# Kernel tuning notes

Measured on AMD Instinct MI355X. Metric: run time of the kernel, lower is better.

Reference implementation:

```python
import jax, jax.numpy as jnp
import jax.numpy.linalg as jnla
import numpy as np
from jax import lax
from jax.scipy.special import polygamma, betainc
import jax.scipy.stats as jaxstats

N, K, L = 2000, 10, 10000   # samples, covariates, cis variants
R = 200                     # max_perm_direct
MAX_ITER_BETA = 100         # max_iter_beta
STEPSIZE, TOL = 1.0, 1e-3


def setup_inputs() -> dict:
    key = jax.random.key(0)
    kx, ky, kg, kp = jax.random.split(key, 4)
    return {
        "X": jax.random.normal(kx, (N, K), jnp.float32),
        "y": jax.random.normal(ky, (N,), jnp.float32),
        "G": jax.random.normal(kg, (N, L), jnp.float32),
        "obs_p": jax.random.uniform(kp, (L,), jnp.float32),
        "offset_eta": jnp.zeros((N,), jnp.float32),
        "seed": 0,
    }


def _beta_loglik(params, p):
    return jnp.sum(jaxstats.beta.logpdf(p, params[0], params[1]))


def _info_and_christoffel(params, n_obs):
    k, n = params[0], params[1]
    pg_1k = polygamma(1, k); pg_1n = polygamma(1, n); pg_1kn = polygamma(1, k + n)
    pg_2k = polygamma(2, k); pg_2n = polygamma(2, n); pg_2kn = polygamma(2, k + n)
    i_kn = -pg_1kn
    i_k = pg_1k + i_kn
    i_n = pg_1n + i_kn
    info_mat = -n_obs * jnp.array([[i_k, i_kn], [i_kn, i_n]])
    i_kkn = pg_1n * pg_2kn
    i_k = -pg_1n * pg_2k + i_kkn + pg_1kn * pg_2k
    i_knn = i_kkn - pg_1kn * pg_2n
    i_nnk = pg_1k * pg_2kn
    i_nkk = i_nnk - pg_1kn * pg_2k
    i_n = -pg_1k * pg_2n + i_nnk + pg_1kn * pg_2n
    scale = -pg_1k * pg_1n + (pg_1k + pg_1n) * pg_1kn
    sec_gamma = 0.5 * jnp.array([[[i_k, i_kkn], [i_kkn, i_knn]],
                                 [[i_nkk, i_nnk], [i_nnk, i_n]]]) / scale
    return info_mat, sec_gamma


def _infer_beta(p_perm, init, max_iter):
    # Newton-Raphson with Christoffel correction; fixed-length scan with an
    # 'active' freeze mask (reverse-differentiable equivalent of the while_loop).
    score_fn = jax.grad(_beta_loglik)
    n_obs = p_perm.shape[0]

    def step(carry, _):
        old_lik, diff, num_iter, old_param = carry
        active = jnp.logical_and(jnp.abs(diff) > TOL, num_iter <= max_iter)
        info_mat, gamma = _info_and_christoffel(old_param, n_obs)
        direction = jnla.solve(info_mat, score_fn(old_param, p_perm))
        adjustment = jnp.einsum('cab,a,b->c', gamma, direction, direction)
        new_param = old_param - STEPSIZE * direction - 0.5 * STEPSIZE ** 2 * adjustment
        new_lik = _beta_loglik(new_param, p_perm)
        new_diff = old_lik - new_lik
        carry = (jnp.where(active, new_lik, old_lik),
                 jnp.where(active, new_diff, diff),
                 jnp.where(active, num_iter + 1, num_iter),
                 jnp.where(active, new_param, old_param))
        return carry, None

    init_c = (jnp.float32(10000.0), jnp.float32(1000.0), jnp.int32(0), init)
    (lik, diff, num_iters, params), _ = lax.scan(step, init_c, None, length=max_iter + 1)
    converged = jnp.logical_and(jnp.abs(diff) < TOL, num_iters <= max_iter).astype(jnp.float32)
    return jnp.array([params[0], params[1], converged])


def _beta_perm(X, y, G, obs_p, offset_eta, seed):
    key = jax.random.key(seed)
    XtX = X.T @ X                               # [K,K]
    Gt = G - X @ jnla.solve(XtX, X.T @ G)       # variants residualized on covariates [N,L]
    gg = jnp.sum(Gt * Gt, axis=0)               # [L]
    dof = N - K - 1

    def perm_step(k, _):
        k, p_key = jax.random.split(k)
        y_p = jax.random.permutation(p_key, y, axis=0) - offset_eta
        yt = y_p - X @ jnla.solve(XtX, X.T @ y_p)   # residualized phenotype [N]
        gy = Gt.T @ y_p                             # == Gt.T @ yt since Gt perp X
        beta = gy / gg
        rss = jnp.sum(yt * yt) - beta * beta * gg   # per-variant residual SS [L]
        se = jnp.sqrt(rss / dof / gg)
        return k, jnp.max(jnp.abs(beta / se))

    _, TS = lax.scan(perm_step, key, None, length=R)          # [R] lead |Z| stats
    p_perm = 1.0 - jaxstats.chi2.cdf(jnp.square(TS), 1.0)     # pval_from_Zstat, dof=1
    p_mean, p_var = jnp.mean(p_perm), jnp.var(p_perm)
    k_init = p_mean * (p_mean * (1.0 - p_mean) / p_var - 1.0)
    n_init = k_init * (1.0 / p_mean - 1.0)
    beta_res = _infer_beta(p_perm, jnp.array([k_init, n_init]), MAX_ITER_BETA)
    # _calc_adjp_beta: Beta CDF of the strongest nominal p-value
    adj_p = betainc(beta_res[0], beta_res[1], jnp.min(obs_p))
    return adj_p, beta_res


def reference(X, y, G, obs_p, offset_eta, seed):
    return _beta_perm(X, y, G, obs_p, offset_eta, seed)
```

## Files before the change

### kernel.cpp

```cpp
#include <hip/hip_runtime.h>
#include <stdint.h>

#ifndef JAX_THREEFRY_PARTITIONABLE
#define JAX_THREEFRY_PARTITIONABLE 1
#endif

#define N_SAMP 2000
#define L_VAR  10000
#define R_PERM 200
#define DOF_D  1989.0

#define KPAD   2048
#define LPAD   10048
#define RPAD   256

#define OFF_PKEYS  0UL
#define OFF_MI     1664UL
#define OFF_MINP   2464UL
#define OFF_XT     2560UL
#define OFF_XTGP   82560UL
#define OFF_GGP    2082560UL
#define OFF_GG     2282560UL
#define OFF_YTY    2322560UL
#define OFF_S      2323392UL
#define OFF_YT     2324224UL
#define WS_OLD     3924224UL
#define OFF_GGP2   82560UL
#define OFF_RGG    725632UL
#define OFF_YHI    2324224UL
#define OFF_XTGP2  3924224UL
#define OFF_YLO    10354944UL
#define OFF_GTHI   11403520UL
#define OFF_GTLO   52560128UL
#define WS_BIG     95186432UL

typedef __attribute__((ext_vector_type(8))) short short8v;
typedef __attribute__((ext_vector_type(4))) float float4v;

__device__ __forceinline__ uint32_t rotl32(uint32_t v, int d) {
  return (v << d) | (v >> (32 - d));
}
__device__ __forceinline__ uint2 tf2(uint32_t k0, uint32_t k1, uint32_t x0, uint32_t x1) {
  uint32_t ks2 = k0 ^ k1 ^ 0x1BD11BDAu;
  x0 += k0; x1 += k1;
#define TF4(a,b,c,d) \
  x0 += x1; x1 = rotl32(x1,a); x1 ^= x0; \
  x0 += x1; x1 = rotl32(x1,b); x1 ^= x0; \
  x0 += x1; x1 = rotl32(x1,c); x1 ^= x0; \
  x0 += x1; x1 = rotl32(x1,d); x1 ^= x0;
  TF4(13,15,26,6)  x0 += k1;  x1 += ks2 + 1u;
  TF4(17,29,16,24) x0 += ks2; x1 += k0 + 2u;
  TF4(13,15,26,6)  x0 += k0;  x1 += k1 + 3u;
  TF4(17,29,16,24) x0 += k1;  x1 += ks2 + 4u;
  TF4(13,15,26,6)  x0 += ks2; x1 += k0 + 5u;
#undef TF4
  return make_uint2(x0, x1);
}

__device__ __forceinline__ void gen_pkeys(const int* seedp, unsigned* pkeys) {
  uint32_t khi = 0u, klo = (uint32_t)(*seedp);
  for (int r = 0; r < R_PERM; ++r) {
#if JAX_THREEFRY_PARTITIONABLE
    uint2 pk = tf2(khi, klo, 0u, 1u);
    uint2 nk = tf2(khi, klo, 0u, 0u);
#else
    uint2 t0 = tf2(khi, klo, 0u, 2u);
    uint2 t1 = tf2(khi, klo, 1u, 3u);
    uint2 nk = make_uint2(t0.x, t1.x);
    uint2 pk = make_uint2(t0.y, t1.y);
#endif
    pkeys[2 * r] = pk.x; pkeys[2 * r + 1] = pk.y;
    khi = nk.x; klo = nk.y;
  }
}

__device__ __forceinline__ double breduce_add(double v, double* red, int tid) {
  red[tid] = v; __syncthreads();
  for (int off = 128; off > 0; off >>= 1) {
    if (tid < off) red[tid] += red[tid + off];
    __syncthreads();
  }
  double r = red[0]; __syncthreads();
  return r;
}

__device__ double dg_digamma(double x) {
  if (!(x > 0.0)) return __builtin_nan("");
  double r = 0.0;
  while (x < 8.0) { r -= 1.0 / x; x += 1.0; }
  double t = 1.0 / x, t2 = t * t;
  double ser = t2 * (1.0/12.0 - t2*(1.0/120.0 - t2*(1.0/252.0 - t2*(1.0/240.0 - t2*(1.0/132.0)))));
  return r + log(x) - 0.5 * t - ser;
}
__device__ double dg_trigamma(double x) {
  if (!(x > 0.0)) return __builtin_nan("");
  double r = 0.0;
  while (x < 8.0) { r += 1.0 / (x * x); x += 1.0; }
  double t = 1.0 / x, t2 = t * t;
  double P = 1.0/6.0 - t2*(1.0/30.0 - t2*(1.0/42.0 - t2*(1.0/30.0 - t2*(5.0/66.0))));
  return r + t + 0.5 * t2 + t * t2 * P;
}
__device__ double dg_tetragamma(double x) {
  if (!(x > 0.0)) return __builtin_nan("");
  double r = 0.0;
  while (x < 8.0) { r -= 2.0 / (x * x * x); x += 1.0; }
  double t = 1.0 / x, t2 = t * t;
  double Q = 1.0 + t + 0.5*t2 - t2*t2*(1.0/6.0 - t2*(1.0/6.0 - t2*(3.0/10.0)));
  return r - t2 * Q;
}
__device__ double betacf_d(double a, double b, double x) {
  const double FPMIN = 1e-300, EPS = 3e-16;
  double qab = a + b, qap = a + 1.0, qam = a - 1.0;
  double c = 1.0, d = 1.0 - qab * x / qap;
  if (fabs(d) < FPMIN) d = FPMIN;
  d = 1.0 / d; double h = d;
  for (int m = 1; m <= 300; ++m) {
    int m2 = 2 * m;
    double aa = m * (b - m) * x / ((qam + m2) * (a + m2));
    d = 1.0 + aa * d; if (fabs(d) < FPMIN) d = FPMIN;
    c = 1.0 + aa / c; if (fabs(c) < FPMIN) c = FPMIN;
    d = 1.0 / d; double del = d * c; h *= del;
    aa = -(a + m) * (qab + m) * x / ((a + m2) * (qap + m2));
    d = 1.0 + aa * d; if (fabs(d) < FPMIN) d = FPMIN;
    c = 1.0 + aa / c; if (fabs(c) < FPMIN) c = FPMIN;
    d = 1.0 / d; del = d * c; h *= del;
    if (fabs(del - 1.0) < EPS) break;
  }
  return h;
}
__device__ double betainc_d(double a, double b, double x) {
  if (!(x > 0.0)) return 0.0;
  if (x >= 1.0) return 1.0;
  double lnbt = lgamma(a + b) - lgamma(a) - lgamma(b) + a * log(x) + b * log1p(-x);
  double bt = exp(lnbt);
  if (x < (a + 1.0) / (a + b + 2.0)) return bt * betacf_d(a, b, x) / a;
  else return 1.0 - bt * betacf_d(b, a, 1.0 - x) / b;
}

__device__ __forceinline__ void fill_keys(unsigned long long* arr, uint32_t kx, uint32_t ky,
                                          int tid, int nthr) {
#if JAX_THREEFRY_PARTITIONABLE
  for (int i = tid; i < 2048; i += nthr) {
    if (i < 2000) {
      uint2 o = tf2(kx, ky, 0u, (uint32_t)i);
      uint32_t bits = o.x ^ o.y;
      arr[i] = (((unsigned long long)bits) << 11) | (unsigned long long)i;
    } else {
      arr[i] = ~0ull;
    }
  }
#else
  for (int j = tid; j < 1024; j += nthr) {
    if (j < 1000) {
      uint2 o = tf2(kx, ky, (uint32_t)j, (uint32_t)(1000 + j));
      arr[j]        = (((unsigned long long)o.x) << 11) | (unsigned long long)j;
      arr[1000 + j] = (((unsigned long long)o.y) << 11) | (unsigned long long)(1000 + j);
    }
  }
  for (int i = 2000 + tid; i < 2048; i += nthr) arr[i] = ~0ull;
#endif
}

__device__ __forceinline__ void tri_ab(int q, int& a, int& b) {
  int aa = 0, rem = q;
  while (rem >= 10 - aa) { rem -= 10 - aa; ++aa; }
  a = aa; b = aa + rem;
}

__device__ __forceinline__ void bf16split(float f, unsigned short& h, unsigned short& l) {
  unsigned u = __float_as_uint(f);
  h = (unsigned short)(u >> 16);
  float rem = f - __uint_as_float(u & 0xFFFF0000u);
  l = (unsigned short)(__float_as_uint(rem) >> 16);
}

__global__ __launch_bounds__(256) void k1_setup(
    const float* __restrict__ X, const float* __restrict__ obs_p,
    float* __restrict__ Xt, double* __restrict__ Mi, float* __restrict__ minp,
    unsigned short* __restrict__ yhi, unsigned short* __restrict__ ylo) {
  int tid = threadIdx.x;
  if (blockIdx.x == 0) {
    __shared__ double wsum[4][55];
    __shared__ double xtx_sh[55];
    __shared__ double A[10][21];
    __shared__ int piv_sh;
    __shared__ double pv_sh;
    int wave = tid >> 6, lane = tid & 63;

    double acc[55];
    #pragma unroll
    for (int q = 0; q < 55; ++q) acc[q] = 0.0;
    for (int i = tid; i < N_SAMP; i += 256) {
      float xv[10];
      #pragma unroll
      for (int k = 0; k < 5; ++k) {
        float2 t2 = *(const float2*)(X + i * 10 + 2 * k);
        xv[2 * k] = t2.x; xv[2 * k + 1] = t2.y;
      }
      int q = 0;
      #pragma unroll
      for (int a = 0; a < 10; ++a)
        #pragma unroll
        for (int b = a; b < 10; ++b)
          acc[q++] += (double)xv[a] * (double)xv[b];
    }
    #pragma unroll
    for (int q = 0; q < 55; ++q) {
      double v = acc[q];
      #pragma unroll
      for (int off = 32; off > 0; off >>= 1) v += __shfl_xor(v, off, 64);
      if (lane == 0) wsum[wave][q] = v;
    }
    __syncthreads();
    if (tid < 55) xtx_sh[tid] = wsum[0][tid] + wsum[1][tid] + wsum[2][tid] + wsum[3][tid];
    __syncthreads();

    if (tid < 200) {
      int r = tid / 20, j = tid % 20;
      double v;
      if (j < 10) {
        int a = r < j ? r : j;
        int b = r < j ? j : r;
        int q = 10 * a - a * (a - 1) / 2 + (b - a);
        v = xtx_sh[q];
      } else {
        v = (j - 10 == r) ? 1.0 : 0.0;
      }
      A[r][j] = v;
    }
    __syncthreads();
    int r_ = tid / 20, j_ = tid % 20;
    bool in200 = (tid < 200);
    for (int c = 0; c < 10; ++c) {
      if (tid == 0) {
        int piv = c; double best = fabs(A[c][c]);
        for (int r2 = c + 1; r2 < 10; ++r2)
          if (fabs(A[r2][c]) > best) { best = fabs(A[r2][c]); piv = r2; }
        piv_sh = piv;
      }
      __syncthreads();
      int piv = piv_sh;
      if (piv != c && tid < 20) {
        double t = A[c][tid]; A[c][tid] = A[piv][tid]; A[piv][tid] = t;
      }
      __syncthreads();
      if (tid == 0) pv_sh = A[c][c];
      __syncthreads();
      if (tid < 20) A[c][tid] *= (1.0 / pv_sh);
      __syncthreads();
      double f = 0.0, acj = 0.0;
      bool act = in200 && (r_ != c);
      if (act) { f = A[r_][c]; acj = A[c][j_]; }
      __syncthreads();
      if (act) A[r_][j_] -= f * acj;
      __syncthreads();
    }
    if (tid < 100) Mi[tid] = A[tid / 10][10 + (tid % 10)];
  } else if (blockIdx.x == 1) {
    __shared__ float redf[256];
    float m = 1e30f;
    for (int i = tid; i < L_VAR; i += 256) m = fminf(m, obs_p[i]);
    redf[tid] = m; __syncthreads();
    for (int off = 128; off > 0; off >>= 1) {
      if (tid < off) redf[tid] = fminf(redf[tid], redf[tid + off]);
      __syncthreads();
    }
    if (tid == 0) *minp = redf[0];
  } else if (blockIdx.x == 2) {
    for (int idx = tid; idx < 10 * N_SAMP; idx += 256) {
      int k = idx / N_SAMP, i = idx - k * N_SAMP;
      Xt[idx] = X[i * 10 + k];
    }
  } else {
    if (yhi) {
      int row = R_PERM + (blockIdx.x - 3);
      size_t base = (size_t)row * KPAD;
      for (int i = tid; i < KPAD; i += 256) {
        yhi[base + i] = 0;
        ylo[base + i] = 0;
      }
    }
  }
}

__global__ __launch_bounds__(256) void k2_xtg(
    const float* __restrict__ G, const float* __restrict__ X,
    const int* __restrict__ seedp, float* __restrict__ XtGp,
    float* __restrict__ GGp, unsigned* __restrict__ pkeys) {
  if (blockIdx.x == 40) {
    if (blockIdx.y == 0 && threadIdx.x == 0) gen_pkeys(seedp, pkeys);
    return;
  }
  int l = blockIdx.x * 256 + threadIdx.x;
  bool valid = (l < L_VAR);
  int i0 = blockIdx.y * 400;
  float acc[10];
  #pragma unroll
  for (int k = 0; k < 10; ++k) acc[k] = 0.f;
  float g2 = 0.f;
  for (int i = i0; i < i0 + 400; ++i) {
    float g = valid ? G[(size_t)i * L_VAR + l] : 0.f;
    #pragma unroll
    for (int k = 0; k < 10; ++k) acc[k] = fmaf(g, X[i * 10 + k], acc[k]);
    g2 = fmaf(g, g, g2);
  }
  if (valid) {
    int part = blockIdx.y;
    #pragma unroll
    for (int k = 0; k < 10; ++k)
      XtGp[((size_t)part * 10 + k) * L_VAR + l] = acc[k];
    GGp[(size_t)part * L_VAR + l] = g2;
  }
}

__global__ __launch_bounds__(256) void k2t_pass(
    const float* __restrict__ G, const float* __restrict__ X,
    const int* __restrict__ seedp,
    unsigned short* __restrict__ GTHI, unsigned short* __restrict__ GTLO,
    float* __restrict__ XtGp2, float* __restrict__ GGp2,
    unsigned* __restrict__ pkeys) {
  if (blockIdx.x == 157) {
    if (blockIdx.y == 0 && threadIdx.x < 2) {
      int t = threadIdx.x;
      uint32_t khi = 0u, klo = (uint32_t)(*seedp);
#if JAX_THREEFRY_PARTITIONABLE
      for (int r = 0; r < R_PERM; ++r) {
        uint2 res = tf2(khi, klo, 0u, (uint32_t)t);
        if (t == 1) { pkeys[2 * r] = res.x; pkeys[2 * r + 1] = res.y; }
        khi = __shfl(res.x, 0, 64);
        klo = __shfl(res.y, 0, 64);
      }
#else
      if (t == 0) gen_pkeys(seedp, pkeys);
#endif
    }
    return;
  }
  __shared__ float T[128][69];
  __shared__ float Xsh[128][10];
  int tid = threadIdx.x;
  int l0 = blockIdx.x * 64, i0 = blockIdx.y * 128;
  for (int it = 0; it < 8; ++it) {
    int fi = it * 256 + tid;
    int row = fi >> 4, c4 = (fi & 15) * 4;
    int i = i0 + row, l = l0 + c4;
    float4 v = make_float4(0.f, 0.f, 0.f, 0.f);
    if (i < N_SAMP && l + 3 < L_VAR) v = *(const float4*)(G + (size_t)i * L_VAR + l);
    T[row][c4 + 0] = v.x; T[row][c4 + 1] = v.y; T[row][c4 + 2] = v.z; T[row][c4 + 3] = v.w;
  }
  for (int q = 0; q < 5; ++q) {
    int idx = q * 256 + tid;
    if (idx < 1280) {
      int row = idx / 10, k = idx - row * 10;
      int i = i0 + row;
      Xsh[row][k] = (i < N_SAMP) ? X[i * 10 + k] : 0.f;
    }
  }
  __syncthreads();
  {
    int w = tid >> 6, lam = tid & 63;
    int half = lam >> 5, i4 = (lam & 31) * 4;
    for (int g = 0; g < 8; ++g) {
      int lloc = g * 8 + w * 2 + half;
      float fv[4];
      fv[0] = T[i4 + 0][lloc]; fv[1] = T[i4 + 1][lloc];
      fv[2] = T[i4 + 2][lloc]; fv[3] = T[i4 + 3][lloc];
      ushort4 hv, lv;
      bf16split(fv[0], hv.x, lv.x);
      bf16split(fv[1], hv.y, lv.y);
      bf16split(fv[2], hv.z, lv.z);
      bf16split(fv[3], hv.w, lv.w);
      size_t idx = (size_t)(l0 + lloc) * KPAD + i0 + i4;
      *(ushort4*)(GTHI + idx) = hv;
      *(ushort4*)(GTLO + idx) = lv;
    }
  }
  int lc = tid & 63, iq = tid >> 6;
  float accx[10];
  #pragma unroll
  for (int k = 0; k < 10; ++k) accx[k] = 0.f;
  float g2 = 0.f;
  for (int j = 0; j < 32; ++j) {
    int i = iq * 32 + j;
    float tv = T[i][lc];
    g2 = fmaf(tv, tv, g2);
    #pragma unroll
    for (int k = 0; k < 10; ++k) accx[k] = fmaf(tv, Xsh[i][k], accx[k]);
  }
  __syncthreads();
  float* scr = &T[0][0];
  #pragma unroll
  for (int k = 0; k < 10; ++k) scr[(iq * 64 + lc) * 10 + k] = accx[k];
  scr[2560 + iq * 64 + lc] = g2;
  __syncthreads();
  for (int idx = tid; idx < 640; idx += 256) {
    int l = idx / 10, k = idx - l * 10;
    float t = scr[(0 * 64 + l) * 10 + k] + scr[(1 * 64 + l) * 10 + k]
            + scr[(2 * 64 + l) * 10 + k] + scr[(3 * 64 + l) * 10 + k];
    XtGp2[((size_t)blockIdx.y * 10 + k) * LPAD + l0 + l] = t;
  }
  if (tid < 64) {
    float s4 = scr[2560 + tid] + scr[2560 + 64 + tid] + scr[2560 + 128 + tid] + scr[2560 + 192 + tid];
    GGp2[(size_t)blockIdx.y * LPAD + l0 + tid] = s4;
  }
}

__global__ __launch_bounds__(256) void k3_gg(
    const float* __restrict__ XtGp, const float* __restrict__ GGp,
    const double* __restrict__ Mi, float* __restrict__ gg) {
  int l = blockIdx.x * 256 + threadIdx.x;
  if (l >= L_VAR) return;
  double t[10]; double g2 = 0.0;
  #pragma unroll
  for (int k = 0; k < 10; ++k) t[k] = 0.0;
  for (int part = 0; part < 5; ++part) {
    #pragma unroll
    for (int k = 0; k < 10; ++k)
      t[k] += (double)XtGp[((size_t)part * 10 + k) * L_VAR + l];
    g2 += (double)GGp[(size_t)part * L_VAR + l];
  }
  double corr = 0.0;
  #pragma unroll
  for (int k = 0; k < 10; ++k) {
    double a = 0.0;
    #pragma unroll
    for (int j = 0; j < 10; ++j) a += Mi[k * 10 + j] * t[j];
    corr += a * t[k];
  }
  gg[l] = (float)(g2 - corr);
}

__global__ __launch_bounds__(256) void k3t_gg(
    const float* __restrict__ XtGp2, const float* __restrict__ GGp2,
    const double* __restrict__ Mi, float* __restrict__ gg, float* __restrict__ rgg) {
  int l = blockIdx.x * 256 + threadIdx.x;
  if (l >= LPAD) return;
  double t[10]; double g2 = 0.0;
  #pragma unroll
  for (int k = 0; k < 10; ++k) t[k] = 0.0;
  for (int part = 0; part < 16; ++part) {
    #pragma unroll
    for (int k = 0; k < 10; ++k)
      t[k] += (double)XtGp2[((size_t)part * 10 + k) * LPAD + l];
    g2 += (double)GGp2[(size_t)part * LPAD + l];
  }
  double corr = 0.0;
  #pragma unroll
  for (int k = 0; k < 10; ++k) {
    double a = 0.0;
    #pragma unroll
    for (int j = 0; j < 10; ++j) a += Mi[k * 10 + j] * t[j];
    corr += a * t[k];
  }
  double v = g2 - corr;
  if (l < L_VAR) {
    gg[l] = (float)v;
    rgg[l] = (v > 0.0) ? (float)(1.0 / v) : 0.f;
  } else {
    rgg[l] = 0.f;
  }
}

__global__ __launch_bounds__(1024) void k4_perm(
    const float* __restrict__ y, const float* __restrict__ offs,
    const float* __restrict__ Xt, const unsigned* __restrict__ pkeys,
    const double* __restrict__ Mi, float* __restrict__ Yt,
    float* __restrict__ yty, unsigned* __restrict__ s,
    unsigned short* __restrict__ yhi, unsigned short* __restrict__ ylo) {
  __shared__ unsigned long long arrA[2048];
  __shared__ unsigned long long arrB[2048];
  __shared__ float yp[2000];
  __shared__ double redL[16][10];
  __shared__ double wf[10];
  __shared__ double red16[16];
  __shared__ double mvd[10];
  __shared__ unsigned ksh[4];
  const int NT = 1024;
  int r = blockIdx.x, tid = threadIdx.x;
  int wid = tid >> 6, lane = tid & 63;

  if (tid == 0) {
    uint32_t phi = pkeys[2 * r], plo = pkeys[2 * r + 1];
#if JAX_THREEFRY_PARTITIONABLE
    uint2 sub1 = tf2(phi, plo, 0u, 1u);
    uint2 key1 = tf2(phi, plo, 0u, 0u);
    uint2 sub2 = tf2(key1.x, key1.y, 0u, 1u);
#else
    uint2 a0 = tf2(phi, plo, 0u, 2u), a1 = tf2(phi, plo, 1u, 3u);
    uint2 key1 = make_uint2(a0.x, a1.x);
    uint2 sub1 = make_uint2(a0.y, a1.y);
    uint2 b0 = tf2(key1.x, key1.y, 0u, 2u), b1 = tf2(key1.x, key1.y, 1u, 3u);
    uint2 sub2 = make_uint2(b0.y, b1.y);
#endif
    ksh[0] = sub1.x; ksh[1] = sub1.y; ksh[2] = sub2.x; ksh[3] = sub2.y;
  }
  __syncthreads();
  uint32_t s1x = ksh[0], s1y = ksh[1], s2x = ksh[2], s2y = ksh[3];

  fill_keys(arrA, s1x, s1y, tid, NT);
  fill_keys(arrB, s2x, s2y, tid, NT);

  for (int size = 2; size <= 2048; size <<= 1) {
    for (int stride = size >> 1; stride > 0; stride >>= 1) {
      __syncthreads();
      int i = 2 * tid - (tid & (stride - 1));
      int j = i + stride;
      bool up = ((i & size) == 0);
      unsigned long long a = arrA[i], b = arrA[j];
      unsigned long long c = arrB[i], d = arrB[j];
      bool swA = up ? (a > b) : (a < b);
      bool swB = up ? (c > d) : (c < d);
      if (swA) { arrA[i] = b; arrA[j] = a; }
      if (swB) { arrB[i] = d; arrB[j] = c; }
    }
  }
  __syncthreads();

  for (int i = tid; i < N_SAMP; i += NT) {
    int s2i = (int)(arrB[i] & 2047u);
    int fin = (int)(arrA[s2i] & 2047u);
    yp[i] = y[fin] - offs[i];
  }
  __syncthreads();

  double wloc[10];
  #pragma unroll
  for (int k = 0; k < 10; ++k) wloc[k] = 0.0;
  for (int i = tid; i < N_SAMP; i += NT) {
    double v = (double)yp[i];
    #pragma unroll
    for (int k = 0; k < 10; ++k) wloc[k] += (double)Xt[k * N_SAMP + i] * v;
  }
  #pragma unroll
  for (int k = 0; k < 10; ++k) {
    double v = wloc[k];
    #pragma unroll
    for (int off = 32; off > 0; off >>= 1) v += __shfl_xor(v, off, 64);
    if (lane == 0) redL[wid][k] = v;
  }
  __syncthreads();
  if (tid < 10) {
    double t = 0.0;
    for (int w2 = 0; w2 < 16; ++w2) t += redL[w2][tid];
    wf[tid] = t;
  }
  __syncthreads();
  if (tid < 10) {
    double m = 0.0;
    #pragma unroll
    for (int k = 0; k < 10; ++k) m += Mi[tid * 10 + k] * wf[k];
    mvd[tid] = m;
  }
  __syncthreads();

  double acc = 0.0;
  for (int i = tid; i < N_SAMP; i += NT) {
    double d = (double)yp[i];
    #pragma unroll
    for (int k = 0; k < 10; ++k) d -= (double)Xt[k * N_SAMP + i] * mvd[k];
    float v = (float)d;
    if (Yt) Yt[(size_t)r * N_SAMP + i] = v;
    yp[i] = v;
    acc += (double)v * (double)v;
  }
  #pragma unroll
  for (int off = 32; off > 0; off >>= 1) acc += __shfl_xor(acc, off, 64);
  if (lane == 0) red16[wid] = acc;
  __syncthreads();
  if (tid == 0) {
    double tot = 0.0;
    for (int w2 = 0; w2 < 16; ++w2) tot += red16[w2];
    yty[r] = (float)tot;
    s[r] = 0u;
  }

  __syncthreads();
  if (yhi) {
    for (int i = tid; i < KPAD; i += NT) {
      float v = (i < N_SAMP) ? yp[i] : 0.f;
      unsigned short h, l;
      bf16split(v, h, l);
      yhi[(size_t)r * KPAD + i] = h;
      ylo[(size_t)r * KPAD + i] = l;
    }
  }
}

__global__ __launch_bounds__(256) void k5_gemm(
    const float* __restrict__ G, const float* __restrict__ Yt,
    const float* __restrict__ gg, unsigned* __restrict__ s) {
  __shared__ float As[16][64];
  __shared__ float Bs[16][68];
  int tid = threadIdx.x;
  int tx = tid & 15, ty = tid >> 4;
  int l0 = blockIdx.x * 64, r0 = blockIdx.y * 64;
  int a_row = tid >> 4;
  int a_col = (tid & 15) * 4;
  int b_row = tid >> 2;
  int b_col = (tid & 3) * 4;
  int gl = l0 + a_col;
  bool aval = (gl < L_VAR);
  int gr = r0 + b_row;
  bool bval = (gr < R_PERM);
  const float* gbase = G + (size_t)a_row * L_VAR + gl;
  const float* ybase = Yt + (size_t)gr * N_SAMP + b_col;

  float4 aR = aval ? *(const float4*)gbase : make_float4(0.f, 0.f, 0.f, 0.f);
  float4 bR = bval ? *(const float4*)ybase : make_float4(0.f, 0.f, 0.f, 0.f);

  float acc[4][4];
  #pragma unroll
  for (int u = 0; u < 4; ++u)
    #pragma unroll
    for (int v = 0; v < 4; ++v) acc[u][v] = 0.f;

  for (int i0 = 0; i0 < N_SAMP; i0 += 16) {
    *(float4*)&As[a_row][a_col] = aR;
    Bs[b_col + 0][b_row] = bR.x;
    Bs[b_col + 1][b_row] = bR.y;
    Bs[b_col + 2][b_row] = bR.z;
    Bs[b_col + 3][b_row] = bR.w;
    __syncthreads();
    int inext = i0 + 16;
    if (inext < N_SAMP) {
      aR = aval ? *(const float4*)(gbase + (size_t)inext * L_VAR) : make_float4(0.f, 0.f, 0.f, 0.f);
      bR = bval ? *(const float4*)(ybase + inext) : make_float4(0.f, 0.f, 0.f, 0.f);
    }
    #pragma unroll
    for (int k = 0; k < 16; ++k) {
      float4 av = *(const float4*)&As[k][tx * 4];
      float4 bv = *(const float4*)&Bs[k][ty * 4];
      float a4[4] = {av.x, av.y, av.z, av.w};
      float b4[4] = {bv.x, bv.y, bv.z, bv.w};
      #pragma unroll
      for (int u = 0; u < 4; ++u)
        #pragma unroll
        for (int v = 0; v < 4; ++v)
          acc[u][v] = fmaf(a4[u], b4[v], acc[u][v]);
    }
    __syncthreads();
  }
  #pragma unroll
  for (int v = 0; v < 4; ++v) {
    int rr = r0 + ty * 4 + v;
    float m = 0.f;
    #pragma unroll
    for (int u = 0; u < 4; ++u) {
      int ll = l0 + tx * 4 + u;
      if (ll < L_VAR) {
        float U = acc[u][v];
        float t = U * U / gg[ll];
        m = fmaxf(m, t);
      }
    }
    #pragma unroll
    for (int off = 8; off > 0; off >>= 1) m = fmaxf(m, __shfl_xor(m, off, 64));
    if (tx == 0 && rr < R_PERM) atomicMax(&s[rr], __float_as_uint(m));
  }
}

__device__ __forceinline__ void k5f_stage(
    int w, int lane, int kb, int l0, int rbase,
    const unsigned short* __restrict__ GTHI, const unsigned short* __restrict__ GTLO,
    const unsigned short* __restrict__ YHI, const unsigned short* __restrict__ YLO,
    unsigned short* Ah, unsigned short* Al, unsigned short* Bh, unsigned short* Bl) {
  int sub = lane >> 2, kq = lane & 3;
  #pragma unroll
  for (int j = 0; j < 6; ++j) {
    int c = w * 6 + j;
    const unsigned short* src;
    unsigned short* dst;
    if (c < 4) {
      src = GTHI + (size_t)(l0 + c * 16 + sub) * KPAD + kb + kq * 8;
      dst = Ah + c * 512 + lane * 8;
    } else if (c < 8) {
      src = GTLO + (size_t)(l0 + (c - 4) * 16 + sub) * KPAD + kb + kq * 8;
      dst = Al + (c - 4) * 512 + lane * 8;
    } else if (c < 16) {
      src = YHI + (size_t)(rbase + (c - 8) * 16 + sub) * KPAD + kb + kq * 8;
      dst = Bh + (c - 8) * 512 + lane * 8;
    } else {
      src = YLO + (size_t)(rbase + (c - 16) * 16 + sub) * KPAD + kb + kq * 8;
      dst = Bl + (c - 16) * 512 + lane * 8;
    }
    __builtin_amdgcn_global_load_lds(
        (const __attribute__((address_space(1))) unsigned int*)(const void*)src,
        (__attribute__((address_space(3))) unsigned int*)(void*)dst, 16, 0, 0);
  }
}

__global__ __launch_bounds__(256) void k5f_mfma(
    const unsigned short* __restrict__ GTHI, const unsigned short* __restrict__ GTLO,
    const unsigned short* __restrict__ YHI, const unsigned short* __restrict__ YLO,
    const float* __restrict__ rgg, unsigned* __restrict__ s) {
  __shared__ unsigned short Ah[3][64 * 32];
  __shared__ unsigned short Al[3][64 * 32];
  __shared__ unsigned short Bh[3][128 * 32];
  __shared__ unsigned short Bl[3][128 * 32];
  int tid = threadIdx.x;
  int w = tid >> 6, lane = tid & 63;
  int row16 = lane & 15, quad = lane >> 4;
  int ltile = blockIdx.x >> 1;
  int rhalf = blockIdx.x & 1;
  int l0 = ltile * 64;
  int rbase = rhalf * 128;

  float4v acc[4][2];
  #pragma unroll
  for (int mt = 0; mt < 4; ++mt)
    #pragma unroll
    for (int nt = 0; nt < 2; ++nt)
      acc[mt][nt] = (float4v){0.f, 0.f, 0.f, 0.f};

  k5f_stage(w, lane, 0,  l0, rbase, GTHI, GTLO, YHI, YLO, Ah[0], Al[0], Bh[0], Bl[0]);
  k5f_stage(w, lane, 32, l0, rbase, GTHI, GTLO, YHI, YLO, Ah[1], Al[1], Bh[1], Bl[1]);
  k5f_stage(w, lane, 64, l0, rbase, GTHI, GTLO, YHI, YLO, Ah[2], Al[2], Bh[2], Bl[2]);

  #pragma unroll 1
  for (int step = 0; step < 64; ++step) {
    int cur = step % 3;
    if (step < 62) {
      asm volatile("s_waitcnt vmcnt(12)" ::: "memory");
    } else if (step == 62) {
      asm volatile("s_waitcnt vmcnt(6)" ::: "memory");
    } else {
      asm volatile("s_waitcnt vmcnt(0)" ::: "memory");
    }
    __builtin_amdgcn_s_barrier();
    __builtin_amdgcn_sched_barrier(0);

    short8v ahf[4], alf[4], bhf[2], blf[2];
    #pragma unroll
    for (int mt = 0; mt < 4; ++mt) {
      int o = (mt * 16 + row16) * 32 + quad * 8;
      ahf[mt] = *(const short8v*)&Ah[cur][o];
      alf[mt] = *(const short8v*)&Al[cur][o];
    }
    #pragma unroll
    for (int nt = 0; nt < 2; ++nt) {
      int o = (w * 32 + nt * 16 + row16) * 32 + quad * 8;
      bhf[nt] = *(const short8v*)&Bh[cur][o];
      blf[nt] = *(const short8v*)&Bl[cur][o];
    }
    #pragma unroll
    for (int nt = 0; nt < 2; ++nt) {
      #pragma unroll
      for (int mt = 0; mt < 4; ++mt) {
        acc[mt][nt] = __builtin_amdgcn_mfma_f32_16x16x32_bf16(ahf[mt], bhf[nt], acc[mt][nt], 0, 0, 0);
        acc[mt][nt] = __builtin_amdgcn_mfma_f32_16x16x32_bf16(ahf[mt], blf[nt], acc[mt][nt], 0, 0, 0);
        acc[mt][nt] = __builtin_amdgcn_mfma_f32_16x16x32_bf16(alf[mt], bhf[nt], acc[mt][nt], 0, 0, 0);
      }
    }
    __builtin_amdgcn_s_barrier();
    if (step + 3 < 64)
      k5f_stage(w, lane, (step + 3) * 32, l0, rbase, GTHI, GTLO, YHI, YLO,
                Ah[cur], Al[cur], Bh[cur], Bl[cur]);
  }

  float rl_[4][4];
  #pragma unroll
  for (int mt = 0; mt < 4; ++mt)
    #pragma unroll
    for (int q = 0; q < 4; ++q)
      rl_[mt][q] = rgg[l0 + mt * 16 + quad * 4 + q];
  #pragma unroll
  for (int nt = 0; nt < 2; ++nt) {
    float m = 0.f;
    #pragma unroll
    for (int mt = 0; mt < 4; ++mt)
      #pragma unroll
      for (int q = 0; q < 4; ++q) {
        float U = acc[mt][nt][q];
        m = fmaxf(m, U * U * rl_[mt][q]);
      }
    m = fmaxf(m, __shfl_xor(m, 16, 64));
    m = fmaxf(m, __shfl_xor(m, 32, 64));
    int r = rbase + w * 32 + nt * 16 + row16;
    if (quad == 0 && r < R_PERM) atomicMax(&s[r], __float_as_uint(m));
  }
}

__global__ __launch_bounds__(256) void k6_final(
    const unsigned* __restrict__ sbits, const float* __restrict__ yty,
    const float* __restrict__ minp, float* __restrict__ out) {
  __shared__ double red[256];
  int tid = threadIdx.x;
  double p = 0.0, p2 = 0.0, lp = 0.0, l1p = 0.0;
  if (tid < R_PERM) {
    double t = (double)__uint_as_float(sbits[tid]);
    double Y = (double)yty[tid];
    double ts2 = DOF_D * t / (Y - t);
    double pp = erfc(sqrt(0.5 * ts2));
    p = pp; p2 = pp * pp; lp = log(pp); l1p = log1p(-pp);
  }
  double Sp  = breduce_add(p, red, tid);
  double Sp2 = breduce_add(p2, red, tid);
  double S1  = breduce_add(lp, red, tid);
  double S2  = breduce_add(l1p, red, tid);
  if (tid < 64) {
    const double nobs = (double)R_PERM;
    double mean = Sp / nobs;
    double var = Sp2 / nobs - mean * mean;
    double k = mean * (mean * (1.0 - mean) / var - 1.0);
    double n = k * (1.0 / mean - 1.0);
    double old_lik = 10000.0, diff = 1000.0;
    int iter = 0;
    int sel = tid % 3, grp = tid / 3;
    while (fabs(diff) > 1e-3 && iter <= 100) {
      double arg = (sel == 0) ? k : (sel == 1) ? n : (k + n);
      double v = 0.0;
      if (grp == 0) v = dg_trigamma(arg);
      else if (grp == 1) v = dg_tetragamma(arg);
      else if (grp == 2) v = dg_digamma(arg);
      double pg1k = __shfl(v, 0, 64), pg1n = __shfl(v, 1, 64), pg1kn = __shfl(v, 2, 64);
      double pg2k = __shfl(v, 3, 64), pg2n = __shfl(v, 4, 64), pg2kn = __shfl(v, 5, 64);
      double dgk  = __shfl(v, 6, 64), dgn  = __shfl(v, 7, 64), dgkn  = __shfl(v, 8, 64);
      double i_kn = -pg1kn, i_k = pg1k + i_kn, i_n = pg1n + i_kn;
      double A = -nobs * i_k, B = -nobs * i_kn, C = -nobs * i_n;
      double s0 = S1 - nobs * (dgk - dgkn);
      double s1 = S2 - nobs * (dgn - dgkn);
      double det = A * C - B * B;
      double d0 = (C * s0 - B * s1) / det;
      double d1 = (A * s1 - B * s0) / det;
      double i_kkn = pg1n * pg2kn;
      double g_k = -pg1n * pg2k + i_kkn + pg1kn * pg2k;
      double i_knn = i_kkn - pg1kn * pg2n;
      double i_nnk = pg1k * pg2kn;
      double i_nkk = i_nnk - pg1kn * pg2k;
      double g_n = -pg1k * pg2n + i_nnk + pg1kn * pg2n;
      double scale = -pg1k * pg1n + (pg1k + pg1n) * pg1kn;
      double f = 0.5 / scale;
      double adj0 = f * (g_k * d0 * d0 + 2.0 * i_kkn * d0 * d1 + i_knn * d1 * d1);
      double adj1 = f * (i_nkk * d0 * d0 + 2.0 * i_nnk * d0 * d1 + g_n * d1 * d1);
      double nk_ = k - d0 - 0.5 * adj0;
      double nn_ = n - d1 - 0.5 * adj1;
      double arg2 = (tid == 0) ? nk_ : (tid == 1) ? nn_ : (nk_ + nn_);
      double lg = (tid < 3) ? lgamma(arg2) : 0.0;
      double lgk = __shfl(lg, 0, 64), lgn = __shfl(lg, 1, 64), lgkn = __shfl(lg, 2, 64);
      double nl = (nk_ - 1.0) * S1 + (nn_ - 1.0) * S2 - nobs * (lgk + lgn - lgkn);
      diff = old_lik - nl;
      old_lik = nl; k = nk_; n = nn_; ++iter;
    }
    if (tid == 0) {
      double conv = (fabs(diff) < 1e-3 && iter <= 100) ? 1.0 : 0.0;
      double adj = betainc_d(k, n, (double)(*minp));
      out[0] = (float)adj;
      out[1] = (float)k;
      out[2] = (float)n;
      out[3] = (float)conv;
    }
  }
}

__global__ void k_err(float* out) {
  if (threadIdx.x < 4) out[threadIdx.x] = -12345.0f;
}

extern "C" void kernel_launch(void* const* d_in, const int* in_sizes, int n_in,
                              void* d_out, int out_size, void* d_ws, size_t ws_size,
                              hipStream_t stream) {
  const float* X     = (const float*)d_in[0];
  const float* y     = (const float*)d_in[1];
  const float* G     = (const float*)d_in[2];
  const float* obs_p = (const float*)d_in[3];
  const float* offs  = (const float*)d_in[4];
  const int*   seedp = (const int*)d_in[5];
  float* out = (float*)d_out;

  if (ws_size < WS_OLD) {
    k_err<<<1, 64, 0, stream>>>(out);
    return;
  }
  char* ws = (char*)d_ws;
  unsigned* pkeys = (unsigned*)(ws + OFF_PKEYS);
  double*   Mi    = (double*)(ws + OFF_MI);
  float*    minp  = (float*)(ws + OFF_MINP);
  float*    Xt    = (float*)(ws + OFF_XT);
  float*    XtGp  = (float*)(ws + OFF_XTGP);
  float*    GGp   = (float*)(ws + OFF_GGP);
  float*    gg    = (float*)(ws + OFF_GG);
  float*    yty   = (float*)(ws + OFF_YTY);
  unsigned* s     = (unsigned*)(ws + OFF_S);
  float*    Yt    = (float*)(ws + OFF_YT);

  bool big = (ws_size >= WS_BIG);
  float*          rgg   = big ? (float*)(ws + OFF_RGG) : nullptr;
  unsigned short* yhi   = big ? (unsigned short*)(ws + OFF_YHI) : nullptr;
  unsigned short* ylo   = big ? (unsigned short*)(ws + OFF_YLO) : nullptr;
  float*          XtGp2 = big ? (float*)(ws + OFF_XTGP2) : nullptr;
  float*          GGp2  = big ? (float*)(ws + OFF_GGP2) : nullptr;
  unsigned short* GTHI  = big ? (unsigned short*)(ws + OFF_GTHI) : nullptr;
  unsigned short* GTLO  = big ? (unsigned short*)(ws + OFF_GTLO) : nullptr;

  if (big) {
    k1_setup<<<3 + (RPAD - R_PERM), 256, 0, stream>>>(X, obs_p, Xt, Mi, minp, yhi, ylo);
    k2t_pass<<<dim3(158, 16), 256, 0, stream>>>(G, X, seedp, GTHI, GTLO, XtGp2, GGp2, pkeys);
    k3t_gg<<<40, 256, 0, stream>>>(XtGp2, GGp2, Mi, gg, rgg);
    k4_perm<<<R_PERM, 1024, 0, stream>>>(y, offs, Xt, pkeys, Mi, nullptr, yty, s, yhi, ylo);
    k5f_mfma<<<314, 256, 0, stream>>>(GTHI, GTLO, yhi, ylo, rgg, s);
  } else {
    k1_setup<<<3, 256, 0, stream>>>(X, obs_p, Xt, Mi, minp, nullptr, nullptr);
    k2_xtg<<<dim3(41, 5), 256, 0, stream>>>(G, X, seedp, XtGp, GGp, pkeys);
    k3_gg<<<40, 256, 0, stream>>>(XtGp, GGp, Mi, gg);
    k4_perm<<<R_PERM, 1024, 0, stream>>>(y, offs, Xt, pkeys, Mi, Yt, yty, s, nullptr, nullptr);
    k5_gemm<<<dim3(157, 4), 256, 0, stream>>>(G, Yt, gg, s);
  }
  k6_final<<<1, 256, 0, stream>>>(s, yty, minp, out);
}
```

Measured before the change: 305.0 us.

## Use wavefront shuffles for bitonic sort stages in permutation kernel

Replaces the fully shared-memory bitonic sort of permutation keys with a register-resident version: each thread holds two keys, intra-wavefront strides use cross-lane shuffles and the pair step is done in registers. Only strides of 128 and above go through LDS with block barriers. This cuts the number of __syncthreads and LDS round-trips per permutation, at the cost of more intricate direction logic that must exactly match the original sort order.

```diff
diff --git a/kernel.cpp b/kernel.cpp
--- a/kernel.cpp
+++ b/kernel.cpp
@@ -137,30 +137,6 @@
   else return 1.0 - bt * betacf_d(b, a, 1.0 - x) / b;
 }
 
-__device__ __forceinline__ void fill_keys(unsigned long long* arr, uint32_t kx, uint32_t ky,
-                                          int tid, int nthr) {
-#if JAX_THREEFRY_PARTITIONABLE
-  for (int i = tid; i < 2048; i += nthr) {
-    if (i < 2000) {
-      uint2 o = tf2(kx, ky, 0u, (uint32_t)i);
-      uint32_t bits = o.x ^ o.y;
-      arr[i] = (((unsigned long long)bits) << 11) | (unsigned long long)i;
-    } else {
-      arr[i] = ~0ull;
-    }
-  }
-#else
-  for (int j = tid; j < 1024; j += nthr) {
-    if (j < 1000) {
-      uint2 o = tf2(kx, ky, (uint32_t)j, (uint32_t)(1000 + j));
-      arr[j]        = (((unsigned long long)o.x) << 11) | (unsigned long long)j;
-      arr[1000 + j] = (((unsigned long long)o.y) << 11) | (unsigned long long)(1000 + j);
-    }
-  }
-  for (int i = 2000 + tid; i < 2048; i += nthr) arr[i] = ~0ull;
-#endif
-}
-
 __device__ __forceinline__ void tri_ab(int q, int& a, int& b) {
   int aa = 0, rem = q;
   while (rem >= 10 - aa) { rem -= 10 - aa; ++aa; }
@@ -172,6 +148,20 @@
   h = (unsigned short)(u >> 16);
   float rem = f - __uint_as_float(u & 0xFFFF0000u);
   l = (unsigned short)(__float_as_uint(rem) >> 16);
+}
+
+__device__ __forceinline__ unsigned long long keyfor(uint32_t kx, uint32_t ky, int e) {
+  if (e >= N_SAMP) return ~0ull;
+#if JAX_THREEFRY_PARTITIONABLE
+  uint2 o = tf2(kx, ky, 0u, (uint32_t)e);
+  uint32_t bits = o.x ^ o.y;
+  return (((unsigned long long)bits) << 11) | (unsigned long long)e;
+#else
+  uint2 o = (e < 1000) ? tf2(kx, ky, (uint32_t)e, (uint32_t)(1000 + e))
+                       : tf2(kx, ky, (uint32_t)(e - 1000), (uint32_t)e);
+  uint32_t bits = (e < 1000) ? o.x : o.y;
+  return (((unsigned long long)bits) << 11) | (unsigned long long)e;
+#endif
 }
 
 __global__ __launch_bounds__(256) void k1_setup(
@@ -461,6 +451,19 @@
   }
 }
 
+#define CEX(v, s, up) { \
+  unsigned long long o_ = __shfl_xor((v), (s), 64); \
+  bool lower_ = ((lane & (s)) == 0); \
+  bool mn_ = (lower_ == (up)); \
+  unsigned long long lo_ = ((v) < o_) ? (v) : o_; \
+  unsigned long long hi_ = ((v) < o_) ? o_ : (v); \
+  (v) = mn_ ? lo_ : hi_; }
+
+#define CEXP(v0, v1, up) { \
+  unsigned long long lo_ = ((v0) < (v1)) ? (v0) : (v1); \
+  unsigned long long hi_ = ((v0) < (v1)) ? (v1) : (v0); \
+  (v0) = (up) ? lo_ : hi_; (v1) = (up) ? hi_ : lo_; }
+
 __global__ __launch_bounds__(1024) void k4_perm(
     const float* __restrict__ y, const float* __restrict__ offs,
     const float* __restrict__ Xt, const unsigned* __restrict__ pkeys,
@@ -486,40 +489,83 @@
     uint2 key1 = tf2(phi, plo, 0u, 0u);
     uint2 sub2 = tf2(key1.x, key1.y, 0u, 1u);
 #else
-    uint2 a0 = tf2(phi, plo, 0u, 2u), a1 = tf2(phi, plo, 1u, 3u);
-    uint2 key1 = make_uint2(a0.x, a1.x);
-    uint2 sub1 = make_uint2(a0.y, a1.y);
-    uint2 b0 = tf2(key1.x, key1.y, 0u, 2u), b1 = tf2(key1.x, key1.y, 1u, 3u);
-    uint2 sub2 = make_uint2(b0.y, b1.y);
+    uint2 a0k = tf2(phi, plo, 0u, 2u), a1k = tf2(phi, plo, 1u, 3u);
+    uint2 key1 = make_uint2(a0k.x, a1k.x);
+    uint2 sub1 = make_uint2(a0k.y, a1k.y);
+    uint2 b0k = tf2(key1.x, key1.y, 0u, 2u), b1k = tf2(key1.x, key1.y, 1u, 3u);
+    uint2 sub2 = make_uint2(b0k.y, b1k.y);
 #endif
     ksh[0] = sub1.x; ksh[1] = sub1.y; ksh[2] = sub2.x; ksh[3] = sub2.y;
   }
   __syncthreads();
   uint32_t s1x = ksh[0], s1y = ksh[1], s2x = ksh[2], s2y = ksh[3];
 
-  fill_keys(arrA, s1x, s1y, tid, NT);
-  fill_keys(arrB, s2x, s2y, tid, NT);
-
-  for (int size = 2; size <= 2048; size <<= 1) {
-    for (int stride = size >> 1; stride > 0; stride >>= 1) {
+  int e0 = 128 * wid + lane;
+  int e1 = e0 + 64;
+  unsigned long long a0 = keyfor(s1x, s1y, e0), a1 = keyfor(s1x, s1y, e1);
+  unsigned long long b0 = keyfor(s2x, s2y, e0), b1 = keyfor(s2x, s2y, e1);
+
+  #pragma unroll
+  for (int size = 2; size <= 32; size <<= 1) {
+    for (int st = size >> 1; st > 0; st >>= 1) {
+      bool up = ((lane & size) == 0);
+      CEX(a0, st, up); CEX(a1, st, up);
+      CEX(b0, st, up); CEX(b1, st, up);
+    }
+  }
+  #pragma unroll
+  for (int st = 32; st > 0; st >>= 1) {
+    CEX(a0, st, true);  CEX(b0, st, true);
+    CEX(a1, st, false); CEX(b1, st, false);
+  }
+  {
+    bool up = ((wid & 1) == 0);
+    CEXP(a0, a1, up); CEXP(b0, b1, up);
+    #pragma unroll
+    for (int st = 32; st > 0; st >>= 1) {
+      CEX(a0, st, up); CEX(a1, st, up);
+      CEX(b0, st, up); CEX(b1, st, up);
+    }
+  }
+  for (int size = 256; size <= 2048; size <<= 1) {
+    arrA[e0] = a0; arrA[e1] = a1;
+    arrB[e0] = b0; arrB[e1] = b1;
+    __syncthreads();
+    for (int st = size >> 1; st >= 128; st >>= 1) {
+      int i = 2 * tid - (tid & (st - 1));
+      int j = i + st;
+      bool up2 = ((i & size) == 0);
+      unsigned long long x0 = arrA[i], x1 = arrA[j];
+      unsigned long long z0 = arrB[i], z1 = arrB[j];
+      bool swA = up2 ? (x0 > x1) : (x0 < x1);
+      bool swB = up2 ? (z0 > z1) : (z0 < z1);
+      if (swA) { arrA[i] = x1; arrA[j] = x0; }
+      if (swB) { arrB[i] = z1; arrB[j] = z0; }
       __syncthreads();
-      int i = 2 * tid - (tid & (stride - 1));
-      int j = i + stride;
-      bool up = ((i & size) == 0);
-      unsigned long long a = arrA[i], b = arrA[j];
-      unsigned long long c = arrB[i], d = arrB[j];
-      bool swA = up ? (a > b) : (a < b);
-      bool swB = up ? (c > d) : (c < d);
-      if (swA) { arrA[i] = b; arrA[j] = a; }
-      if (swB) { arrB[i] = d; arrB[j] = c; }
-    }
-  }
-  __syncthreads();
-
-  for (int i = tid; i < N_SAMP; i += NT) {
-    int s2i = (int)(arrB[i] & 2047u);
-    int fin = (int)(arrA[s2i] & 2047u);
-    yp[i] = y[fin] - offs[i];
+    }
+    a0 = arrA[e0]; a1 = arrA[e1];
+    b0 = arrB[e0]; b1 = arrB[e1];
+    bool up = (((unsigned)(128 * wid) & (unsigned)size) == 0);
+    CEXP(a0, a1, up); CEXP(b0, b1, up);
+    #pragma unroll
+    for (int st = 32; st > 0; st >>= 1) {
+      CEX(a0, st, up); CEX(a1, st, up);
+      CEX(b0, st, up); CEX(b1, st, up);
+    }
+  }
+
+  arrA[e0] = a0; arrA[e1] = a1;
+  __syncthreads();
+
+  {
+    int s2i0 = (int)(b0 & 2047u);
+    int fin0 = (int)(arrA[s2i0] & 2047u);
+    yp[e0] = y[fin0] - offs[e0];
+    if (e1 < N_SAMP) {
+      int s2i1 = (int)(b1 & 2047u);
+      int fin1 = (int)(arrA[s2i1] & 2047u);
+      yp[e1] = y[fin1] - offs[e1];
+    }
   }
   __syncthreads();
 
```

Result: faster. 297.9 us (-2.3%).
